# Kernel tuning notes

Measured on AMD Instinct MI355X. Metric: run time of the kernel, lower is better.

The kernel has to match this reference:

```python
import jax, jax.numpy as jnp
import numpy as np

NUM_HEADS = 8
FOCUSING_FACTOR = 3.0
EPS = 1e-6


def setup_inputs() -> dict:
    key = jax.random.key(0)
    ks = jax.random.split(key, 5)
    B, C, H, W = 16, 256, 64, 64
    hd = C // NUM_HEADS
    return {
        "x": jax.random.normal(ks[0], (B, C, H, W), jnp.float32),
        "qkv_w": jax.random.normal(ks[1], (3 * C, C), jnp.float32) * 0.02,
        "qkv_b": jnp.zeros((3 * C,), jnp.float32),
        "proj_w": jax.random.normal(ks[2], (C, C), jnp.float32) * 0.02,
        "proj_b": jnp.zeros((C,), jnp.float32),
        "dwc_w": jax.random.normal(ks[3], (hd, 1, 5, 5), jnp.float32) * 0.02,
        "dwc_b": jnp.zeros((hd,), jnp.float32),
        "scale": jnp.zeros((1, 1, C), jnp.float32),
    }


def reference(x, qkv_w, qkv_b, proj_w, proj_b, dwc_w, dwc_b, scale):
    B, C, H, W = x.shape
    N = H * W
    hd = C // NUM_HEADS

    # b c h w -> b (h w) c
    xf = x.reshape(B, C, N).transpose(0, 2, 1)
    qkv = xf @ qkv_w.T + qkv_b  # [B, N, 3C]
    q, k, v = jnp.split(qkv, 3, axis=-1)

    # focusing feature map
    q = jax.nn.relu(q) + EPS
    k = jax.nn.relu(k) + EPS
    sc = jax.nn.softplus(scale)
    q = q / sc
    k = k / sc
    q_norm = jnp.linalg.norm(q, axis=-1, keepdims=True)
    k_norm = jnp.linalg.norm(k, axis=-1, keepdims=True)
    # focusing_factor <= 6 branch
    q = q ** FOCUSING_FACTOR
    k = k ** FOCUSING_FACTOR
    q = q / jnp.linalg.norm(q, axis=-1, keepdims=True) * q_norm
    k = k / jnp.linalg.norm(k, axis=-1, keepdims=True) * k_norm

    # b n (h c) -> (b h) n c
    def to_heads(t):
        return t.reshape(B, N, NUM_HEADS, hd).transpose(0, 2, 1, 3).reshape(B * NUM_HEADS, N, hd)

    q, k, v = to_heads(q), to_heads(k), to_heads(v)

    i, j, c, d = N, N, hd, hd
    z = 1.0 / (jnp.einsum('bic,bc->bi', q, k.sum(axis=1)) + EPS)
    if i * j * (c + d) > c * d * (i + j):
        kv = jnp.einsum('bjc,bjd->bcd', k, v)  # [(BH), c, d]
        out = jnp.einsum('bic,bcd,bi->bid', q, kv, z)
    else:
        qk = jnp.einsum('bic,bjc->bij', q, k)
        out = jnp.einsum('bij,bjd,bi->bid', qk, v, z)

    # depthwise conv on v: b (w h) c -> b c w h (square map)
    num = int(N ** 0.5)
    fm = v.transpose(0, 2, 1).reshape(B * NUM_HEADS, hd, num, num)
    fm = jax.lax.conv_general_dilated(
        fm, dwc_w, window_strides=(1, 1), padding='SAME',
        feature_group_count=hd,
        dimension_numbers=('NCHW', 'OIHW', 'NCHW')) + dwc_b[None, :, None, None]
    fm = fm.reshape(B * NUM_HEADS, hd, N).transpose(0, 2, 1)
    out = out + fm

    # (b h) n c -> b n (h c)
    out = out.reshape(B, NUM_HEADS, N, hd).transpose(0, 2, 1, 3).reshape(B, N, C)
    out = out @ proj_w.T + proj_b
    # b (h w) c -> b c h w
    return out.transpose(0, 2, 1).reshape(B, C, H, W)
```

## Files before the change

### kernel.cpp

```cpp
#include <hip/hip_runtime.h>
#include <cmath>

#define B_   16
#define C_   256
#define HW_  64
#define N_   4096
#define NH_  8
#define HD_  32
#define M_   (B_ * N_)
#define QKVC (3 * C_)
#define EPS_ 1e-6f

typedef short bf16x8 __attribute__((ext_vector_type(8)));
typedef float f32x4 __attribute__((ext_vector_type(4)));
typedef unsigned int u32x4 __attribute__((ext_vector_type(4)));

__device__ __forceinline__ float b2f(unsigned short u) {
  union { unsigned int i; float f; } v;
  v.i = ((unsigned int)u) << 16;
  return v.f;
}
__device__ __forceinline__ float blo(unsigned int u) {
  union { unsigned int i; float f; } v; v.i = u << 16; return v.f;
}
__device__ __forceinline__ float bhi(unsigned int u) {
  union { unsigned int i; float f; } v; v.i = u & 0xffff0000u; return v.f;
}
__device__ __forceinline__ unsigned short f2b(float f) {
  union { float f; unsigned int i; } v;
  v.f = f;
  unsigned int r = v.i + 0x7FFFu + ((v.i >> 16) & 1u);
  return (unsigned short)(r >> 16);
}
__device__ __forceinline__ void gload_lds16(const void* g, void* l) {
  __builtin_amdgcn_global_load_lds(
      (const __attribute__((address_space(1))) void*)g,
      (__attribute__((address_space(3))) void*)l, 16, 0, 0);
}

__global__ __launch_bounds__(256) void k_cast_x(const float* __restrict__ x,
                                                unsigned short* __restrict__ xT) {
  __shared__ float t[32][33];
  const int n0 = blockIdx.x * 32, c0 = blockIdx.y * 32, b = blockIdx.z;
  const int tid = threadIdx.x;
  const int r = tid >> 3, g = (tid & 7) * 4;
  float4 v = *reinterpret_cast<const float4*>(
      &x[((size_t)(b * C_ + c0 + r)) * N_ + n0 + g]);
  t[r][g + 0] = v.x; t[r][g + 1] = v.y; t[r][g + 2] = v.z; t[r][g + 3] = v.w;
  __syncthreads();
  ushort4 o;
  o.x = f2b(t[g + 0][r]); o.y = f2b(t[g + 1][r]);
  o.z = f2b(t[g + 2][r]); o.w = f2b(t[g + 3][r]);
  *reinterpret_cast<ushort4*>(&xT[((size_t)(b * N_ + n0 + r)) * C_ + c0 + g]) = o;
}

__global__ __launch_bounds__(256) void k_cast_w(const float* __restrict__ w1,
                                                const float* __restrict__ w2,
                                                unsigned short* __restrict__ dst) {
  const int g4 = (blockIdx.x * 256 + threadIdx.x) * 4;
  float4 v;
  if (g4 < 196608) v = *reinterpret_cast<const float4*>(w1 + g4);
  else             v = *reinterpret_cast<const float4*>(w2 + (g4 - 196608));
  ushort4 o;
  o.x = f2b(v.x); o.y = f2b(v.y); o.z = f2b(v.z); o.w = f2b(v.w);
  *reinterpret_cast<ushort4*>(dst + g4) = o;
}

__global__ void k_prep_scale(const float* __restrict__ scale,
                             float* __restrict__ rsc) {
  const int c = threadIdx.x;
  rsc[c] = 1.f / log1pf(expf(scale[c]));
}

template <int LDA, int OUTMODE, int NCOL>
__global__ __launch_bounds__(256) void k_gemm(
    const unsigned short* __restrict__ A, const unsigned short* __restrict__ W,
    const float* __restrict__ bias, void* __restrict__ outp) {
  __shared__ unsigned short As[128 * 64];
  __shared__ unsigned short Bs[128 * 64];
  const int tid = threadIdx.x;
  const int wid = tid >> 6, lane = tid & 63;
  const int lin = blockIdx.x + blockIdx.y * 512;
  const int bandp = lin >> 3;
  const int rowb = bandp / NCOL;
  const int colb = bandp - rowb * NCOL;
  const int m0 = (((lin & 7) << 6) + rowb) * 128;
  const int col0 = colb * 128;
  const int wr = wid >> 1, wc = wid & 1;

  const int lrow = lane >> 3;
  const int sl = (lane & 7) ^ (lrow & 7);

  f32x4 acc[4][4];
#pragma unroll
  for (int i = 0; i < 4; ++i)
#pragma unroll
    for (int j = 0; j < 4; ++j) acc[i][j] = (f32x4){0.f, 0.f, 0.f, 0.f};

  for (int kt = 0; kt < 4; ++kt) {
    const int k0 = kt * 64;
#pragma unroll
    for (int q = 0; q < 4; ++q) {
      const int chunk = wid * 4 + q;
      const int row = chunk * 8 + lrow;
      gload_lds16(A + (size_t)(m0 + row) * LDA + k0 + sl * 8, &As[chunk * 512]);
      gload_lds16(W + (size_t)(col0 + row) * 256 + k0 + sl * 8, &Bs[chunk * 512]);
    }
    __syncthreads();

    bf16x8 fa[2][4], fb[2][4];
#pragma unroll
    for (int i = 0; i < 4; ++i) {
      const int ra = wr * 64 + i * 16 + (lane & 15);
      const int rb = wc * 64 + i * 16 + (lane & 15);
#pragma unroll
      for (int ks = 0; ks < 2; ++ks) {
        const int s = ks * 4 + (lane >> 4);
        fa[ks][i] = *reinterpret_cast<const bf16x8*>(
            &As[ra * 64 + ((s ^ (ra & 7)) * 8)]);
        fb[ks][i] = *reinterpret_cast<const bf16x8*>(
            &Bs[rb * 64 + ((s ^ (rb & 7)) * 8)]);
      }
    }
#pragma unroll
    for (int i = 0; i < 4; ++i)
#pragma unroll
      for (int j = 0; j < 4; ++j) {
        acc[i][j] = __builtin_amdgcn_mfma_f32_16x16x32_bf16(fa[0][i], fb[0][j],
                                                            acc[i][j], 0, 0, 0);
        acc[i][j] = __builtin_amdgcn_mfma_f32_16x16x32_bf16(fa[1][i], fb[1][j],
                                                            acc[i][j], 0, 0, 0);
      }
    __syncthreads();
  }

  if (OUTMODE == 0) {
    unsigned short* O = (unsigned short*)outp;
#pragma unroll
    for (int j = 0; j < 4; ++j) {
      const int colg = col0 + wc * 64 + j * 16 + (lane & 15);
      const float bb = bias[colg];
#pragma unroll
      for (int i = 0; i < 4; ++i) {
        const int mrow = m0 + wr * 64 + i * 16 + ((lane >> 4) << 2);
#pragma unroll
        for (int r = 0; r < 4; ++r)
          O[(size_t)(mrow + r) * QKVC + colg] = f2b(acc[i][j][r] + bb);
      }
    }
  } else {
    float* O = (float*)outp;
    const int b = m0 >> 12;
    const int nb0 = (m0 & 4095) + wr * 64;
#pragma unroll
    for (int j = 0; j < 4; ++j) {
      const int colg = col0 + wc * 64 + j * 16 + (lane & 15);
      const float bb = bias[colg];
#pragma unroll
      for (int i = 0; i < 4; ++i) {
        const int nb = nb0 + i * 16 + ((lane >> 4) << 2);
        f32x4 o = acc[i][j];
        o += bb;
        *reinterpret_cast<f32x4*>(&O[((size_t)(b * C_ + colg)) * N_ + nb]) = o;
      }
    }
  }
}

__global__ __launch_bounds__(256) void k_focus(unsigned short* __restrict__ qkv,
                                               const float* __restrict__ rsc) {
  const int wave = threadIdx.x >> 6, lane = threadIdx.x & 63;
  const int t = blockIdx.x * 4 + wave;
  const size_t base = (size_t)t * QKVC + lane * 4;

  uint2 qu = *reinterpret_cast<const uint2*>(qkv + base);
  uint2 ku = *reinterpret_cast<const uint2*>(qkv + base + C_);
  const f32x4 rs = *reinterpret_cast<const f32x4*>(rsc + lane * 4);

  float q[4], k[4], q3[4], k3[4];
  q[0] = blo(qu.x); q[1] = bhi(qu.x); q[2] = blo(qu.y); q[3] = bhi(qu.y);
  k[0] = blo(ku.x); k[1] = bhi(ku.x); k[2] = blo(ku.y); k[3] = bhi(ku.y);

  float sq2 = 0.f, sq6 = 0.f, sk2 = 0.f, sk6 = 0.f;
#pragma unroll
  for (int i = 0; i < 4; ++i) {
    q[i] = (fmaxf(q[i], 0.f) + EPS_) * rs[i];
    k[i] = (fmaxf(k[i], 0.f) + EPS_) * rs[i];
    const float q2 = q[i] * q[i], k2 = k[i] * k[i];
    q3[i] = q2 * q[i];
    k3[i] = k2 * k[i];
    sq2 += q2; sk2 += k2;
    sq6 += q3[i] * q3[i];
    sk6 += k3[i] * k3[i];
  }
#pragma unroll
  for (int off = 1; off < 64; off <<= 1) {
    sq2 += __shfl_xor(sq2, off);
    sq6 += __shfl_xor(sq6, off);
    sk2 += __shfl_xor(sk2, off);
    sk6 += __shfl_xor(sk6, off);
  }
  const float fq = sqrtf(sq2 / sq6);
  const float fk = sqrtf(sk2 / sk6);

  uint2 oq, ok;
  oq.x = (unsigned int)f2b(q3[0] * fq) | ((unsigned int)f2b(q3[1] * fq) << 16);
  oq.y = (unsigned int)f2b(q3[2] * fq) | ((unsigned int)f2b(q3[3] * fq) << 16);
  ok.x = (unsigned int)f2b(k3[0] * fk) | ((unsigned int)f2b(k3[1] * fk) << 16);
  ok.y = (unsigned int)f2b(k3[2] * fk) | ((unsigned int)f2b(k3[3] * fk) << 16);
  *reinterpret_cast<uint2*>(qkv + base) = oq;
  *reinterpret_cast<uint2*>(qkv + base + C_) = ok;
}

#define KVP_CHUNKS 16
__global__ __launch_bounds__(256) void k_kv_part(
    const unsigned short* __restrict__ qkv, float* __restrict__ kvp,
    float* __restrict__ ksp) {
  const int bh = blockIdx.x;
  const int chunk = blockIdx.y;
  const int b = bh >> 3, h = bh & 7;
  const int tid = threadIdx.x;
  __shared__ float ksf[64 * 36];
  __shared__ float vsf[64 * 36];

  const int c = tid >> 3;
  const int d0 = (tid & 7) * 4;
  const int srow = tid >> 2;
  const int sseg = (tid & 3) * 8;
  const int j0 = chunk * 256;

  float a0 = 0.f, a1 = 0.f, a2 = 0.f, a3 = 0.f, ksum = 0.f;

  uint4 ku, vu;
  {
    const size_t rb = ((size_t)(b * N_ + j0 + srow)) * QKVC + h * HD_ + sseg;
    ku = *reinterpret_cast<const uint4*>(qkv + rb + C_);
    vu = *reinterpret_cast<const uint4*>(qkv + rb + 2 * C_);
  }

  for (int t = 0; t < 4; ++t) {
    {
      f32x4 k0 = {blo(ku.x), bhi(ku.x), blo(ku.y), bhi(ku.y)};
      f32x4 k1 = {blo(ku.z), bhi(ku.z), blo(ku.w), bhi(ku.w)};
      f32x4 v0 = {blo(vu.x), bhi(vu.x), blo(vu.y), bhi(vu.y)};
      f32x4 v1 = {blo(vu.z), bhi(vu.z), blo(vu.w), bhi(vu.w)};
      *reinterpret_cast<f32x4*>(&ksf[srow * 36 + sseg]) = k0;
      *reinterpret_cast<f32x4*>(&ksf[srow * 36 + sseg + 4]) = k1;
      *reinterpret_cast<f32x4*>(&vsf[srow * 36 + sseg]) = v0;
      *reinterpret_cast<f32x4*>(&vsf[srow * 36 + sseg + 4]) = v1;
    }
    __syncthreads();
    if (t < 3) {
      const size_t rb =
          ((size_t)(b * N_ + j0 + (t + 1) * 64 + srow)) * QKVC + h * HD_ + sseg;
      ku = *reinterpret_cast<const uint4*>(qkv + rb + C_);
      vu = *reinterpret_cast<const uint4*>(qkv + rb + 2 * C_);
    }
#pragma unroll 8
    for (int jj = 0; jj < 64; ++jj) {
      const float kc = ksf[jj * 36 + c];
      const f32x4 vv = *reinterpret_cast<const f32x4*>(&vsf[jj * 36 + d0]);
      a0 += kc * vv[0];
      a1 += kc * vv[1];
      a2 += kc * vv[2];
      a3 += kc * vv[3];
      ksum += kc;
    }
    __syncthreads();
  }

  float* kvo = kvp + ((size_t)chunk * 128 + bh) * 1024 + c * 32 + d0;
  kvo[0] = a0; kvo[1] = a1; kvo[2] = a2; kvo[3] = a3;
  if ((tid & 7) == 0) ksp[((size_t)chunk * 128 + bh) * 32 + c] = ksum;
}

__global__ __launch_bounds__(256) void k_kv_reduce(
    const float* __restrict__ kvp, const float* __restrict__ ksp,
    float* __restrict__ kv, float* __restrict__ ksum) {
  const int bh = blockIdx.x;
  for (int p = threadIdx.x; p < 1024; p += 256) {
    float s = 0.f;
#pragma unroll
    for (int ch = 0; ch < KVP_CHUNKS; ++ch)
      s += kvp[((size_t)ch * 128 + bh) * 1024 + p];
    kv[bh * 1024 + p] = s;
  }
  if (threadIdx.x < 32) {
    float s = 0.f;
#pragma unroll
    for (int ch = 0; ch < KVP_CHUNKS; ++ch)
      s += ksp[((size_t)ch * 128 + bh) * 32 + threadIdx.x];
    ksum[bh * 32 + threadIdx.x] = s;
  }
}

__global__ __launch_bounds__(256) void k_attn_conv_f(
    unsigned short* __restrict__ qkv, const float* __restrict__ kv,
    const float* __restrict__ ksum, const float* __restrict__ dwc_w,
    const float* __restrict__ dwc_b) {
  const int lin = blockIdx.x;
  const int g2 = (lin & 7) * 256 + (lin >> 3);
  const int bh = g2 >> 4;
  const int ig = g2 & 15;
  const int i0 = ig * 4;
  const int b = bh >> 3, h = bh & 7;
  const int tid = threadIdx.x;
  const int wave = tid >> 6, lane = tid & 63;

  __shared__ float w_s[800];
  __shared__ float b_s[32];
  __shared__ unsigned short v_s[8 * 64 * 32];

#pragma unroll
  for (int rr = 0; rr < 8; ++rr) {
    const int ii = i0 + rr - 2;
    if (ii < 0 || ii >= 64) continue;
    gload_lds16(qkv + ((size_t)(b * N_ + ii * 64 + wave * 16 + (lane >> 2))) * QKVC +
                    2 * C_ + h * HD_ + (lane & 3) * 8,
                &v_s[rr * 2048 + wave * 512]);
  }
  for (int p = tid; p < 800; p += 256)
    w_s[p] = dwc_w[(p & 31) * 25 + (p >> 5)];
  if (tid < 32) b_s[tid] = dwc_b[tid];

  {
    const int kb = (lane >> 4) * 8;
    const int col = lane & 15;
    const float* kvb_row = kv + bh * 1024;
    const float* ksb = ksum + bh * 32;
    bf16x8 bh0, bh1, bl0, bl1;
    float ks0[8];
#pragma unroll
    for (int t = 0; t < 8; ++t) {
      const float v0 = kvb_row[(kb + t) * 32 + col];
      const float v1 = kvb_row[(kb + t) * 32 + col + 16];
      const unsigned short h0 = f2b(v0), h1 = f2b(v1);
      ((unsigned short*)&bh0)[t] = h0;
      ((unsigned short*)&bh1)[t] = h1;
      ((unsigned short*)&bl0)[t] = f2b(v0 - b2f(h0));
      ((unsigned short*)&bl1)[t] = f2b(v1 - b2f(h1));
      ks0[t] = ksb[kb + t];
    }
    const int r0 = (i0 + wave) * 64;
#pragma unroll
    for (int rt = 0; rt < 4; ++rt) {
      const int row = r0 + rt * 16 + (lane & 15);
      const bf16x8 a = *reinterpret_cast<const bf16x8*>(
          qkv + (size_t)(b * N_ + row) * QKVC + h * HD_ + kb);
      float zp = 0.f;
#pragma unroll
      for (int t = 0; t < 8; ++t)
        zp += b2f(((const unsigned short*)&a)[t]) * ks0[t];
      zp += __shfl_xor(zp, 16);
      zp += __shfl_xor(zp, 32);
      const float z = 1.f / (zp + EPS_);

      f32x4 acc0 = {0.f, 0.f, 0.f, 0.f}, acc1 = {0.f, 0.f, 0.f, 0.f};
      acc0 = __builtin_amdgcn_mfma_f32_16x16x32_bf16(a, bl0, acc0, 0, 0, 0);
      acc1 = __builtin_amdgcn_mfma_f32_16x16x32_bf16(a, bl1, acc1, 0, 0, 0);
      acc0 = __builtin_amdgcn_mfma_f32_16x16x32_bf16(a, bh0, acc0, 0, 0, 0);
      acc1 = __builtin_amdgcn_mfma_f32_16x16x32_bf16(a, bh1, acc1, 0, 0, 0);

#pragma unroll
      for (int r = 0; r < 4; ++r) {
        const int rr = (lane >> 4) * 4 + r;
        const float zr = __shfl(z, rr);
        unsigned short* op =
            qkv + (size_t)(b * N_ + r0 + rt * 16 + rr) * QKVC + h * HD_;
        op[col] = f2b(acc0[r] * zr);
        op[col + 16] = f2b(acc1[r] * zr);
      }
    }
  }
  __syncthreads();

  {
    const int j = tid >> 2;
    const int d0 = (tid & 3) * 8;
    float fm[4][8];
#pragma unroll
    for (int r = 0; r < 4; ++r)
#pragma unroll
      for (int dd = 0; dd < 8; ++dd) fm[r][dd] = b_s[d0 + dd];

#pragma unroll
    for (int lr = 0; lr < 8; ++lr) {
      const int ii = i0 + lr - 2;
      if (ii < 0 || ii >= 64) continue;
#pragma unroll
      for (int kj = 0; kj < 5; ++kj) {
        const int jj = j + kj - 2;
        if (jj < 0 || jj >= 64) continue;
        const unsigned int* vr = reinterpret_cast<const unsigned int*>(
            &v_s[lr * 2048 + jj * 32 + d0]);
        float vf[8];
#pragma unroll
        for (int p = 0; p < 4; ++p) {
          const unsigned int vu = vr[p];
          vf[2 * p + 0] = blo(vu);
          vf[2 * p + 1] = bhi(vu);
        }
#pragma unroll
        for (int r = 0; r < 4; ++r) {
          const int kr = lr - r;
          if (kr < 0 || kr > 4) continue;
          const float* wt = &w_s[(kr * 5 + kj) * 32 + d0];
#pragma unroll
          for (int dd = 0; dd < 8; ++dd) fm[r][dd] += vf[dd] * wt[dd];
        }
      }
    }

#pragma unroll
    for (int r = 0; r < 4; ++r) {
      const int i = i0 + r;
      unsigned int* orow = reinterpret_cast<unsigned int*>(
          qkv + ((size_t)(b * N_ + i * 64 + j)) * QKVC + h * HD_ + d0);
      uint4 cur = *reinterpret_cast<const uint4*>(orow);
      unsigned int o[4] = {cur.x, cur.y, cur.z, cur.w};
#pragma unroll
      for (int p = 0; p < 4; ++p) {
        const unsigned int lo = f2b(blo(o[p]) + fm[r][2 * p + 0]);
        const unsigned int hi = f2b(bhi(o[p]) + fm[r][2 * p + 1]);
        o[p] = lo | (hi << 16);
      }
      *reinterpret_cast<uint4*>(orow) = make_uint4(o[0], o[1], o[2], o[3]);
    }
  }
}

extern "C" void kernel_launch(void* const* d_in, const int* in_sizes, int n_in,
                              void* d_out, int out_size, void* d_ws,
                              size_t ws_size, hipStream_t stream) {
  (void)in_sizes; (void)n_in; (void)out_size; (void)ws_size;
  const float* x      = (const float*)d_in[0];
  const float* qkv_w  = (const float*)d_in[1];
  const float* qkv_b  = (const float*)d_in[2];
  const float* proj_w = (const float*)d_in[3];
  const float* proj_b = (const float*)d_in[4];
  const float* dwc_w  = (const float*)d_in[5];
  const float* dwc_b  = (const float*)d_in[6];
  const float* scale  = (const float*)d_in[7];
  float* out = (float*)d_out;

  char* w = (char*)d_ws;
  unsigned short* xT   = (unsigned short*)w; w += (size_t)M_ * C_ * 2;
  unsigned short* qkvb = (unsigned short*)w; w += (size_t)M_ * QKVC * 2;
  unsigned short* wq   = (unsigned short*)w; w += (size_t)(QKVC + C_) * C_ * 2;
  unsigned short* wp   = wq + (size_t)QKVC * C_;
  float* kvp   = (float*)w;                  w += (size_t)KVP_CHUNKS * 128 * 1024 * 4;
  float* ksp   = (float*)w;                  w += (size_t)KVP_CHUNKS * 128 * 32 * 4;
  float* kvb   = (float*)w;                  w += 128 * 1024 * 4;
  float* ksumb = (float*)w;                  w += 128 * 32 * 4;
  float* rscb  = (float*)w;                  w += 256 * 4;

  k_prep_scale<<<1, 256, 0, stream>>>(scale, rscb);
  k_cast_x<<<dim3(N_ / 32, C_ / 32, B_), 256, 0, stream>>>(x, xT);
  k_cast_w<<<256, 256, 0, stream>>>(qkv_w, proj_w, wq);
  k_gemm<256, 0, 6><<<dim3(512, 6), 256, 0, stream>>>(
      xT, wq, qkv_b, (void*)qkvb);
  k_focus<<<M_ / 4, 256, 0, stream>>>(qkvb, rscb);
  k_kv_part<<<dim3(128, KVP_CHUNKS), 256, 0, stream>>>(qkvb, kvp, ksp);
  k_kv_reduce<<<128, 256, 0, stream>>>(kvp, ksp, kvb, ksumb);
  k_attn_conv_f<<<2048, 256, 0, stream>>>(qkvb, kvb, ksumb, dwc_w, dwc_b);
  k_gemm<768, 1, 2><<<dim3(512, 2), 256, 0, stream>>>(
      qkvb, wp, proj_b, (void*)out);
}
```

Before: 195.0 us.

## Fuse focusing feature map with per-chunk KV partial accumulation

Merges the focus kernel and the KV partial-product kernel into one kernel. Each block normalizes q and k for 128 tokens of one batch, writes q back, and accumulates k^T v and the k sum in shared memory without storing k to global memory. This removes one launch and the global round trip of k. In exchange the grid shrinks to 512 blocks that each process rows serially with wave reductions, and the chunk count doubles, which adds work to the reduce step.

```diff
diff --git a/kernel.cpp b/kernel.cpp
--- a/kernel.cpp
+++ b/kernel.cpp
@@ -167,111 +167,93 @@
   }
 }
 
-__global__ __launch_bounds__(256) void k_focus(unsigned short* __restrict__ qkv,
-                                               const float* __restrict__ rsc) {
-  const int wave = threadIdx.x >> 6, lane = threadIdx.x & 63;
-  const int t = blockIdx.x * 4 + wave;
-  const size_t base = (size_t)t * QKVC + lane * 4;
-
-  uint2 qu = *reinterpret_cast<const uint2*>(qkv + base);
-  uint2 ku = *reinterpret_cast<const uint2*>(qkv + base + C_);
+#define KVP_CHUNKS 32
+__global__ __launch_bounds__(256) void k_focus_kv(
+    unsigned short* __restrict__ qkv, const float* __restrict__ rsc,
+    float* __restrict__ kvp, float* __restrict__ ksp) {
+  const int chunk = blockIdx.x;
+  const int b = blockIdx.y;
+  const int tid = threadIdx.x;
+  const int wave = tid >> 6, lane = tid & 63;
+  __shared__ float ksf[16][256];
+  __shared__ float vsf[16][256];
+
   const f32x4 rs = *reinterpret_cast<const f32x4*>(rsc + lane * 4);
-
-  float q[4], k[4], q3[4], k3[4];
-  q[0] = blo(qu.x); q[1] = bhi(qu.x); q[2] = blo(qu.y); q[3] = bhi(qu.y);
-  k[0] = blo(ku.x); k[1] = bhi(ku.x); k[2] = blo(ku.y); k[3] = bhi(ku.y);
-
-  float sq2 = 0.f, sq6 = 0.f, sk2 = 0.f, sk6 = 0.f;
-#pragma unroll
-  for (int i = 0; i < 4; ++i) {
-    q[i] = (fmaxf(q[i], 0.f) + EPS_) * rs[i];
-    k[i] = (fmaxf(k[i], 0.f) + EPS_) * rs[i];
-    const float q2 = q[i] * q[i], k2 = k[i] * k[i];
-    q3[i] = q2 * q[i];
-    k3[i] = k2 * k[i];
-    sq2 += q2; sk2 += k2;
-    sq6 += q3[i] * q3[i];
-    sk6 += k3[i] * k3[i];
-  }
-#pragma unroll
-  for (int off = 1; off < 64; off <<= 1) {
-    sq2 += __shfl_xor(sq2, off);
-    sq6 += __shfl_xor(sq6, off);
-    sk2 += __shfl_xor(sk2, off);
-    sk6 += __shfl_xor(sk6, off);
-  }
-  const float fq = sqrtf(sq2 / sq6);
-  const float fk = sqrtf(sk2 / sk6);
-
-  uint2 oq, ok;
-  oq.x = (unsigned int)f2b(q3[0] * fq) | ((unsigned int)f2b(q3[1] * fq) << 16);
-  oq.y = (unsigned int)f2b(q3[2] * fq) | ((unsigned int)f2b(q3[3] * fq) << 16);
-  ok.x = (unsigned int)f2b(k3[0] * fk) | ((unsigned int)f2b(k3[1] * fk) << 16);
-  ok.y = (unsigned int)f2b(k3[2] * fk) | ((unsigned int)f2b(k3[3] * fk) << 16);
-  *reinterpret_cast<uint2*>(qkv + base) = oq;
-  *reinterpret_cast<uint2*>(qkv + base + C_) = ok;
-}
-
-#define KVP_CHUNKS 16
-__global__ __launch_bounds__(256) void k_kv_part(
-    const unsigned short* __restrict__ qkv, float* __restrict__ kvp,
-    float* __restrict__ ksp) {
-  const int bh = blockIdx.x;
-  const int chunk = blockIdx.y;
-  const int b = bh >> 3, h = bh & 7;
-  const int tid = threadIdx.x;
-  __shared__ float ksf[64 * 36];
-  __shared__ float vsf[64 * 36];
-
-  const int c = tid >> 3;
-  const int d0 = (tid & 7) * 4;
-  const int srow = tid >> 2;
-  const int sseg = (tid & 3) * 8;
-  const int j0 = chunk * 256;
-
-  float a0 = 0.f, a1 = 0.f, a2 = 0.f, a3 = 0.f, ksum = 0.f;
-
-  uint4 ku, vu;
-  {
-    const size_t rb = ((size_t)(b * N_ + j0 + srow)) * QKVC + h * HD_ + sseg;
-    ku = *reinterpret_cast<const uint4*>(qkv + rb + C_);
-    vu = *reinterpret_cast<const uint4*>(qkv + rb + 2 * C_);
-  }
-
-  for (int t = 0; t < 4; ++t) {
-    {
-      f32x4 k0 = {blo(ku.x), bhi(ku.x), blo(ku.y), bhi(ku.y)};
-      f32x4 k1 = {blo(ku.z), bhi(ku.z), blo(ku.w), bhi(ku.w)};
-      f32x4 v0 = {blo(vu.x), bhi(vu.x), blo(vu.y), bhi(vu.y)};
-      f32x4 v1 = {blo(vu.z), bhi(vu.z), blo(vu.w), bhi(vu.w)};
-      *reinterpret_cast<f32x4*>(&ksf[srow * 36 + sseg]) = k0;
-      *reinterpret_cast<f32x4*>(&ksf[srow * 36 + sseg + 4]) = k1;
-      *reinterpret_cast<f32x4*>(&vsf[srow * 36 + sseg]) = v0;
-      *reinterpret_cast<f32x4*>(&vsf[srow * 36 + sseg + 4]) = v1;
+  f32x4 acc8[8];
+#pragma unroll
+  for (int i = 0; i < 8; ++i) acc8[i] = (f32x4){0.f, 0.f, 0.f, 0.f};
+  float ksum = 0.f;
+  const int h = tid >> 5, c = tid & 31;
+  const int j0 = chunk * 128;
+
+  for (int stage = 0; stage < 8; ++stage) {
+#pragma unroll
+    for (int s = 0; s < 4; ++s) {
+      const int srow = wave * 4 + s;
+      const size_t base =
+          ((size_t)(b * N_ + j0 + stage * 16 + srow)) * QKVC + lane * 4;
+      const uint2 qu = *reinterpret_cast<const uint2*>(qkv + base);
+      const uint2 ku = *reinterpret_cast<const uint2*>(qkv + base + C_);
+      const uint2 vu = *reinterpret_cast<const uint2*>(qkv + base + 2 * C_);
+
+      float q[4], k[4], q3[4], k3[4];
+      q[0] = blo(qu.x); q[1] = bhi(qu.x); q[2] = blo(qu.y); q[3] = bhi(qu.y);
+      k[0] = blo(ku.x); k[1] = bhi(ku.x); k[2] = blo(ku.y); k[3] = bhi(ku.y);
+
+      float sq2 = 0.f, sq6 = 0.f, sk2 = 0.f, sk6 = 0.f;
+#pragma unroll
+      for (int i = 0; i < 4; ++i) {
+        q[i] = (fmaxf(q[i], 0.f) + EPS_) * rs[i];
+        k[i] = (fmaxf(k[i], 0.f) + EPS_) * rs[i];
+        const float q2 = q[i] * q[i], k2 = k[i] * k[i];
+        q3[i] = q2 * q[i];
+        k3[i] = k2 * k[i];
+        sq2 += q2; sk2 += k2;
+        sq6 += q3[i] * q3[i];
+        sk6 += k3[i] * k3[i];
+      }
+#pragma unroll
+      for (int off = 1; off < 64; off <<= 1) {
+        sq2 += __shfl_xor(sq2, off);
+        sq6 += __shfl_xor(sq6, off);
+        sk2 += __shfl_xor(sk2, off);
+        sk6 += __shfl_xor(sk6, off);
+      }
+      const float fq = sqrtf(sq2 / sq6);
+      const float fk = sqrtf(sk2 / sk6);
+
+      uint2 oq;
+      oq.x = (unsigned int)f2b(q3[0] * fq) |
+             ((unsigned int)f2b(q3[1] * fq) << 16);
+      oq.y = (unsigned int)f2b(q3[2] * fq) |
+             ((unsigned int)f2b(q3[3] * fq) << 16);
+      *reinterpret_cast<uint2*>(qkv + base) = oq;
+
+      const f32x4 kf = {k3[0] * fk, k3[1] * fk, k3[2] * fk, k3[3] * fk};
+      const f32x4 vf = {blo(vu.x), bhi(vu.x), blo(vu.y), bhi(vu.y)};
+      *reinterpret_cast<f32x4*>(&ksf[srow][lane * 4]) = kf;
+      *reinterpret_cast<f32x4*>(&vsf[srow][lane * 4]) = vf;
     }
     __syncthreads();
-    if (t < 3) {
-      const size_t rb =
-          ((size_t)(b * N_ + j0 + (t + 1) * 64 + srow)) * QKVC + h * HD_ + sseg;
-      ku = *reinterpret_cast<const uint4*>(qkv + rb + C_);
-      vu = *reinterpret_cast<const uint4*>(qkv + rb + 2 * C_);
-    }
-#pragma unroll 8
-    for (int jj = 0; jj < 64; ++jj) {
-      const float kc = ksf[jj * 36 + c];
-      const f32x4 vv = *reinterpret_cast<const f32x4*>(&vsf[jj * 36 + d0]);
-      a0 += kc * vv[0];
-      a1 += kc * vv[1];
-      a2 += kc * vv[2];
-      a3 += kc * vv[3];
+#pragma unroll 4
+    for (int tt = 0; tt < 16; ++tt) {
+      const float kc = ksf[tt][tid];
       ksum += kc;
+      const float* vrow = &vsf[tt][h * 32];
+#pragma unroll
+      for (int d4 = 0; d4 < 8; ++d4) {
+        const f32x4 vv = *reinterpret_cast<const f32x4*>(&vrow[d4 * 4]);
+        acc8[d4] += kc * vv;
+      }
     }
     __syncthreads();
   }
 
-  float* kvo = kvp + ((size_t)chunk * 128 + bh) * 1024 + c * 32 + d0;
-  kvo[0] = a0; kvo[1] = a1; kvo[2] = a2; kvo[3] = a3;
-  if ((tid & 7) == 0) ksp[((size_t)chunk * 128 + bh) * 32 + c] = ksum;
+  float* kvo = kvp + ((size_t)chunk * 128 + b * 8 + h) * 1024 + c * 32;
+#pragma unroll
+  for (int d4 = 0; d4 < 8; ++d4)
+    *reinterpret_cast<f32x4*>(&kvo[d4 * 4]) = acc8[d4];
+  ksp[((size_t)chunk * 128 + b * 8 + h) * 32 + c] = ksum;
 }
 
 __global__ __launch_bounds__(256) void k_kv_reduce(
@@ -459,8 +441,7 @@
   k_cast_w<<<256, 256, 0, stream>>>(qkv_w, proj_w, wq);
   k_gemm<256, 0, 6><<<dim3(512, 6), 256, 0, stream>>>(
       xT, wq, qkv_b, (void*)qkvb);
-  k_focus<<<M_ / 4, 256, 0, stream>>>(qkvb, rscb);
-  k_kv_part<<<dim3(128, KVP_CHUNKS), 256, 0, stream>>>(qkvb, kvp, ksp);
+  k_focus_kv<<<dim3(KVP_CHUNKS, B_), 256, 0, stream>>>(qkvb, rscb, kvp, ksp);
   k_kv_reduce<<<128, 256, 0, stream>>>(kvp, ksp, kvb, ksumb);
   k_attn_conv_f<<<2048, 256, 0, stream>>>(qkvb, kvb, ksumb, dwc_w, dwc_b);
   k_gemm<768, 1, 2><<<dim3(512, 2), 256, 0, stream>>>(
```

Measured after the change: 209.4 us. +7.4%, slower.
